# Optimization experiments

Measured on AMD Instinct MI355X. Metric: run time of the kernel, lower is better.

## Reference

```python
import jax, jax.numpy as jnp
import numpy as np

HEADS = 8
DIM_HEAD = 64
SCALE = DIM_HEAD ** -0.5


def setup_inputs() -> dict:
    key = jax.random.key(0)
    ks = jax.random.split(key, 5)
    B, N, M, D = 8, 1024, 1024, 512
    inner = HEADS * DIM_HEAD  # 512
    return {
        "x": jax.random.normal(ks[0], (B, N, D), dtype=jnp.float32),
        "context": jax.random.normal(ks[1], (B, M, D), dtype=jnp.float32),
        "Wq": jax.random.normal(ks[2], (D, inner), dtype=jnp.float32) * (D ** -0.5),
        "Wkv": jax.random.normal(ks[3], (D, 2 * inner), dtype=jnp.float32) * (D ** -0.5),
        "Wo": jax.random.normal(ks[4], (inner, D), dtype=jnp.float32) * (inner ** -0.5),
        "bo": jnp.zeros((D,), dtype=jnp.float32),
    }


def reference(x, context, Wq, Wkv, Wo, bo):
    B, N, D = x.shape
    M = context.shape[1]
    q = x @ Wq                      # [B, N, inner]
    kv = context @ Wkv              # [B, M, 2*inner]
    k, v = jnp.split(kv, 2, axis=-1)
    # b n (h d) -> b h n d
    split_heads = lambda t: t.reshape(t.shape[0], t.shape[1], HEADS, DIM_HEAD).transpose(0, 2, 1, 3)
    q, k, v = split_heads(q), split_heads(k), split_heads(v)
    dots = jnp.einsum('bhid,bhjd->bhij', q, k) * SCALE  # [B, H, N, M]
    attn = jax.nn.softmax(dots, axis=-1)
    out = jnp.einsum('bhij,bhjd->bhid', attn, v)        # [B, H, N, d]
    out = out.transpose(0, 2, 1, 3).reshape(B, N, HEADS * DIM_HEAD)
    return out @ Wo + bo            # [B, N, D]
```

## Files before the change

### kernel.cpp

```cpp
#include <hip/hip_runtime.h>
#include <stdint.h>

#define LOG2E 1.44269504088896340736f
#define QSCALE (0.125f * LOG2E)

typedef __bf16 bf16x8 __attribute__((ext_vector_type(8)));
typedef float floatx4 __attribute__((ext_vector_type(4)));

__device__ __forceinline__ unsigned short bfbits(float f) {
  __bf16 h = (__bf16)f;
  return __builtin_bit_cast(unsigned short, h);
}

__device__ __forceinline__ float fast_exp2(float x) {
#if __has_builtin(__builtin_amdgcn_exp2f)
  return __builtin_amdgcn_exp2f(x);
#else
  return exp2f(x);
#endif
}

__device__ __forceinline__ void gl2lds16(const void* g, void* l) {
  __builtin_amdgcn_global_load_lds((const __attribute__((address_space(1))) void*)g,
                                   (__attribute__((address_space(3))) void*)l, 16, 0, 0);
}

__global__ __launch_bounds__(256)
void prep_kernel(const float* __restrict__ x, const float* __restrict__ ctx,
                 const float* __restrict__ Wq, const float* __restrict__ Wkv,
                 const float* __restrict__ Wo,
                 unsigned short* __restrict__ Xb, unsigned short* __restrict__ Cb,
                 unsigned short* __restrict__ WqT, unsigned short* __restrict__ WkvT,
                 unsigned short* __restrict__ WoT) {
  int blk = blockIdx.x;
  int tid = threadIdx.x;
  if (blk < 8192) {
    const float* in = blk < 4096 ? x : ctx;
    unsigned short* out = blk < 4096 ? Xb : Cb;
    int i = (((blk & 4095) * 256) + tid) * 4;
    float4 v = *(const float4*)(in + i);
    unsigned long long pk = (unsigned long long)bfbits(v.x)
                          | ((unsigned long long)bfbits(v.y) << 16)
                          | ((unsigned long long)bfbits(v.z) << 32)
                          | ((unsigned long long)bfbits(v.w) << 48);
    *(unsigned long long*)(out + i) = pk;
  } else {
    __shared__ float tile[32][33];
    int t = blk - 8192;
    const float* in; unsigned short* out; int N; int tb;
    if (t < 256)      { in = Wq;  out = WqT;  N = 512;  tb = t; }
    else if (t < 768) { in = Wkv; out = WkvT; N = 1024; tb = t - 256; }
    else              { in = Wo;  out = WoT;  N = 512;  tb = t - 768; }
    const int K = 512;
    int nbx = N / 32;
    int n0 = (tb % nbx) * 32, k0 = (tb / nbx) * 32;
    int tx = tid & 31, ty = tid >> 5;
#pragma unroll
    for (int r = ty; r < 32; r += 8)
      tile[r][tx] = in[(long)(k0 + r) * N + n0 + tx];
    __syncthreads();
#pragma unroll
    for (int r = ty; r < 32; r += 8)
      out[(long)(n0 + r) * K + k0 + tx] = bfbits(tile[tx][r]);
  }
}

__global__ __launch_bounds__(256)
void proj_gemm(const unsigned short* __restrict__ Xb, const unsigned short* __restrict__ Cb,
               const unsigned short* __restrict__ WqT, const unsigned short* __restrict__ WkvT,
               unsigned short* __restrict__ Qb, unsigned short* __restrict__ Kb,
               unsigned short* __restrict__ Vt) {
  __shared__ unsigned short As[128 * 32];
  __shared__ unsigned short Bs[128 * 32];

  int idx = blockIdx.x;
  const unsigned short* A; const unsigned short* Bt;
  long bm, bn; int role;
  if (idx < 256) { role = 0; A = Xb; Bt = WqT;  bn = (long)(idx & 3) * 128; bm = (long)(idx >> 2) * 128; }
  else { idx -= 256; role = 1; A = Cb; Bt = WkvT; bn = (long)(idx & 7) * 128; bm = (long)(idx >> 3) * 128; }

  const int tid = threadIdx.x;
  const int wave = tid >> 6;
  const int lane = tid & 63;
  const int l15 = lane & 15;
  const int q4 = lane >> 4;
  const int wm = (wave & 1) * 64;
  const int wn = (wave >> 1) * 64;
  const int K = 512;

  floatx4 acc[4][4];
#pragma unroll
  for (int i = 0; i < 4; ++i)
#pragma unroll
    for (int j = 0; j < 4; ++j) { acc[i][j][0]=0.f; acc[i][j][1]=0.f; acc[i][j][2]=0.f; acc[i][j][3]=0.f; }

  for (int k0 = 0; k0 < K; k0 += 32) {
#pragma unroll
    for (int cc = 0; cc < 2; ++cc) {
      int c = cc * 256 + tid;
      int r = c >> 2, kc = c & 3;
      gl2lds16(A + (bm + r) * (long)K + k0 + kc * 8, (char*)As + c * 16);
      gl2lds16(Bt + (bn + r) * (long)K + k0 + kc * 8, (char*)Bs + c * 16);
    }
    __syncthreads();
    bf16x8 af[4], bfr[4];
#pragma unroll
    for (int i = 0; i < 4; ++i)
      af[i] = *(const bf16x8*)(As + (wm + i * 16 + l15) * 32 + q4 * 8);
#pragma unroll
    for (int j = 0; j < 4; ++j)
      bfr[j] = *(const bf16x8*)(Bs + (wn + j * 16 + l15) * 32 + q4 * 8);
#pragma unroll
    for (int i = 0; i < 4; ++i)
#pragma unroll
      for (int j = 0; j < 4; ++j)
        acc[i][j] = __builtin_amdgcn_mfma_f32_16x16x32_bf16(af[i], bfr[j], acc[i][j], 0, 0, 0);
    __syncthreads();
  }

  const bool vrole = (role == 1) && (bn >= 512);
#pragma unroll
  for (int i = 0; i < 4; ++i) {
#pragma unroll
    for (int j = 0; j < 4; ++j) {
      long col = bn + wn + j * 16 + l15;
      if (vrole) {
        long h = (col - 512) >> 6, d = col & 63;
        long row0 = bm + wm + i * 16 + q4 * 4;
        long b = row0 >> 10, m0 = row0 & 1023;
        unsigned long long pk = (unsigned long long)bfbits(acc[i][j][0])
                              | ((unsigned long long)bfbits(acc[i][j][1]) << 16)
                              | ((unsigned long long)bfbits(acc[i][j][2]) << 32)
                              | ((unsigned long long)bfbits(acc[i][j][3]) << 48);
        *(unsigned long long*)(Vt + ((b * 8 + h) * 64 + d) * 1024 + m0) = pk;
      } else {
        long h = col >> 6, d = col & 63;
#pragma unroll
        for (int r = 0; r < 4; ++r) {
          long row = bm + wm + i * 16 + q4 * 4 + r;
          long b = row >> 10, n = row & 1023;
          float v = acc[i][j][r];
          if (role == 0) Qb[((b * 8 + h) * 1024 + n) * 64 + d] = bfbits(v * QSCALE);
          else           Kb[((b * 8 + h) * 1024 + n) * 64 + d] = bfbits(v);
        }
      }
    }
  }
}

__global__ __launch_bounds__(256)
void attn_kernel(const unsigned short* __restrict__ Qb,
                 const unsigned short* __restrict__ Kb,
                 const unsigned short* __restrict__ Vt,
                 unsigned short* __restrict__ Ob)
{
  __shared__ unsigned short Ksm[2][4096];
  __shared__ unsigned short Vsm[2][4096];
  __shared__ unsigned short Psm[128 * 64];

  const int tid = threadIdx.x;
  const int wave = tid >> 6;
  const int lane = tid & 63;
  const int l15 = lane & 15;
  const int q4 = lane >> 4;
  const int bh = blockIdx.x;
  const int nb = blockIdx.y;

  const long qrow0 = (long)bh * 1024 + nb * 128 + wave * 32;

  bf16x8 qf[2][2];
#pragma unroll
  for (int qn = 0; qn < 2; ++qn)
#pragma unroll
    for (int ks = 0; ks < 2; ++ks)
      qf[qn][ks] = *(const bf16x8*)(Qb + (qrow0 + qn * 16 + l15) * 64 + ks * 32 + q4 * 8);

  floatx4 acc[2][4];
#pragma unroll
  for (int i = 0; i < 2; ++i)
#pragma unroll
    for (int d = 0; d < 4; ++d) { acc[i][d][0]=0.f; acc[i][d][1]=0.f; acc[i][d][2]=0.f; acc[i][d][3]=0.f; }
  float suml[2] = {0.0f, 0.0f};

  const unsigned short* Kbase = Kb + (long)bh * 65536;
  const unsigned short* Vbase = Vt + (long)bh * 65536;
  int koff[2], voff[2], lds16[2];
#pragma unroll
  for (int cc = 0; cc < 2; ++cc) {
    int c = cc * 256 + tid;
    int jrow = c >> 3;
    int cact = (c & 7) ^ (jrow & 7);
    koff[cc] = jrow * 64 + cact * 8;
    voff[cc] = jrow * 1024 + cact * 8;
    lds16[cc] = c * 16;
  }

  const int s7 = l15 & 7;
  int kfo[2][4];
  int pao[2][2];
  int pwo[2][4];
#pragma unroll
  for (int ks = 0; ks < 2; ++ks) {
#pragma unroll
    for (int jn = 0; jn < 4; ++jn)
      kfo[ks][jn] = (jn * 16 + l15) * 64 + (((ks * 4 + q4) ^ s7) * 8);
#pragma unroll
    for (int i = 0; i < 2; ++i)
      pao[ks][i] = (wave * 32 + i * 16 + l15) * 64 + (((ks * 4 + q4) ^ s7) * 8);
  }
#pragma unroll
  for (int qn = 0; qn < 2; ++qn)
#pragma unroll
    for (int jn = 0; jn < 4; ++jn)
      pwo[qn][jn] = (wave * 32 + qn * 16 + l15) * 64 + (((jn * 2 + (q4 >> 1)) ^ s7) * 8) + (q4 & 1) * 4;

#pragma unroll
  for (int cc = 0; cc < 2; ++cc) {
    gl2lds16(Kbase + koff[cc], (char*)Ksm[0] + lds16[cc]);
    gl2lds16(Vbase + voff[cc], (char*)Vsm[0] + lds16[cc]);
  }

#define ATTN_TILE(TIDX, CUR, STAGE)                                                          \
  {                                                                                          \
    __syncthreads();                                                                         \
    if (STAGE) {                                                                             \
      _Pragma("unroll")                                                                      \
      for (int cc = 0; cc < 2; ++cc) {                                                       \
        gl2lds16(Kbase + ((TIDX) + 1) * 4096 + koff[cc], (char*)Ksm[(CUR) ^ 1] + lds16[cc]); \
        gl2lds16(Vbase + ((TIDX) + 1) * 64 + voff[cc], (char*)Vsm[(CUR) ^ 1] + lds16[cc]);   \
      }                                                                                      \
    }                                                                                        \
    floatx4 st[4][2];                                                                        \
    _Pragma("unroll")                                                                        \
    for (int jn = 0; jn < 4; ++jn)                                                           \
      _Pragma("unroll")                                                                      \
      for (int qn = 0; qn < 2; ++qn) {                                                       \
        st[jn][qn][0] = 0.f; st[jn][qn][1] = 0.f; st[jn][qn][2] = 0.f; st[jn][qn][3] = 0.f;  \
      }                                                                                      \
    _Pragma("unroll")                                                                        \
    for (int ks = 0; ks < 2; ++ks) {                                                         \
      bf16x8 kfr[4];                                                                         \
      _Pragma("unroll")                                                                      \
      for (int jn = 0; jn < 4; ++jn)                                                         \
        kfr[jn] = *(const bf16x8*)(Ksm[(CUR)] + kfo[ks][jn]);                                \
      _Pragma("unroll")                                                                      \
      for (int jn = 0; jn < 4; ++jn)                                                         \
        _Pragma("unroll")                                                                    \
        for (int qn = 0; qn < 2; ++qn)                                                       \
          st[jn][qn] = __builtin_amdgcn_mfma_f32_16x16x32_bf16(kfr[jn], qf[qn][ks],          \
                                                               st[jn][qn], 0, 0, 0);         \
    }                                                                                        \
    _Pragma("unroll")                                                                        \
    for (int qn = 0; qn < 2; ++qn) {                                                         \
      _Pragma("unroll")                                                                      \
      for (int jn = 0; jn < 4; ++jn) {                                                       \
        float p0 = fast_exp2(st[jn][qn][0]);                                                 \
        float p1 = fast_exp2(st[jn][qn][1]);                                                 \
        float p2 = fast_exp2(st[jn][qn][2]);                                                 \
        float p3 = fast_exp2(st[jn][qn][3]);                                                 \
        suml[qn] += (p0 + p1) + (p2 + p3);                                                   \
        unsigned int lo = (unsigned int)bfbits(p0) | ((unsigned int)bfbits(p1) << 16);       \
        unsigned int hi = (unsigned int)bfbits(p2) | ((unsigned int)bfbits(p3) << 16);       \
        unsigned long long pk = (unsigned long long)lo | ((unsigned long long)hi << 32);     \
        *(unsigned long long*)(Psm + pwo[qn][jn]) = pk;                                      \
      }                                                                                      \
    }                                                                                        \
    __asm__ volatile("s_waitcnt lgkmcnt(0)" ::: "memory");                                   \
    _Pragma("unroll")                                                                        \
    for (int ks = 0; ks < 2; ++ks) {                                                         \
      bf16x8 pa[2], vb[4];                                                                   \
      _Pragma("unroll")                                                                      \
      for (int i = 0; i < 2; ++i)                                                            \
        pa[i] = *(const bf16x8*)(Psm + pao[ks][i]);                                          \
      _Pragma("unroll")                                                                      \
      for (int dn = 0; dn < 4; ++dn)                                                         \
        vb[dn] = *(const bf16x8*)(Vsm[(CUR)] + kfo[ks][dn]);                                 \
      _Pragma("unroll")                                                                      \
      for (int i = 0; i < 2; ++i)                                                            \
        _Pragma("unroll")                                                                    \
        for (int dn = 0; dn < 4; ++dn)                                                       \
          acc[i][dn] = __builtin_amdgcn_mfma_f32_16x16x32_bf16(pa[i], vb[dn],                \
                                                               acc[i][dn], 0, 0, 0);         \
    }                                                                                        \
  }

  for (int tt = 0; tt < 8; ++tt) {
    ATTN_TILE(2 * tt, 0, true);
    ATTN_TILE(2 * tt + 1, 1, (tt < 7));
  }
#undef ATTN_TILE

  float inv[2], invr[2][4];
#pragma unroll
  for (int qn = 0; qn < 2; ++qn) {
    float l = suml[qn];
    l += __shfl_xor(l, 16, 64);
    l += __shfl_xor(l, 32, 64);
    inv[qn] = 1.0f / l;
#pragma unroll
    for (int r = 0; r < 4; ++r) invr[qn][r] = __shfl(inv[qn], q4 * 4 + r, 64);
  }

  const int b = bh >> 3, h = bh & 7;
#pragma unroll
  for (int i = 0; i < 2; ++i) {
#pragma unroll
    for (int dn = 0; dn < 4; ++dn) {
#pragma unroll
      for (int r = 0; r < 4; ++r) {
        long row = (long)b * 1024 + nb * 128 + wave * 32 + i * 16 + q4 * 4 + r;
        long col = h * 64 + dn * 16 + l15;
        Ob[row * 512 + col] = bfbits(acc[i][dn][r] * invr[i][r]);
      }
    }
  }
}

__global__ __launch_bounds__(256)
void out_gemm(const unsigned short* __restrict__ A,
              const unsigned short* __restrict__ Bt,
              float* __restrict__ outF, const float* __restrict__ bias) {
  __shared__ unsigned short As[64 * 32];
  __shared__ unsigned short Bs[128 * 32];

  const int tid = threadIdx.x;
  const int wave = tid >> 6;
  const int lane = tid & 63;
  const int l15 = lane & 15;
  const int q4 = lane >> 4;
  const int wm = (wave & 1) * 32;
  const int wn = (wave >> 1) * 64;
  const long bm = (long)blockIdx.y * 64;
  const long bn = (long)blockIdx.x * 128;
  const int K = 512, N = 512;

  floatx4 acc[2][4];
#pragma unroll
  for (int i = 0; i < 2; ++i)
#pragma unroll
    for (int j = 0; j < 4; ++j) { acc[i][j][0]=0.f; acc[i][j][1]=0.f; acc[i][j][2]=0.f; acc[i][j][3]=0.f; }

  for (int k0 = 0; k0 < K; k0 += 32) {
    {
      int r = tid >> 2, kc = tid & 3;
      gl2lds16(A + (bm + r) * (long)K + k0 + kc * 8, (char*)As + tid * 16);
    }
#pragma unroll
    for (int cc = 0; cc < 2; ++cc) {
      int c = cc * 256 + tid;
      int r = c >> 2, kc = c & 3;
      gl2lds16(Bt + (bn + r) * (long)K + k0 + kc * 8, (char*)Bs + c * 16);
    }
    __syncthreads();
    bf16x8 af[2], bfr[4];
#pragma unroll
    for (int i = 0; i < 2; ++i)
      af[i] = *(const bf16x8*)(As + (wm + i * 16 + l15) * 32 + q4 * 8);
#pragma unroll
    for (int j = 0; j < 4; ++j)
      bfr[j] = *(const bf16x8*)(Bs + (wn + j * 16 + l15) * 32 + q4 * 8);
#pragma unroll
    for (int i = 0; i < 2; ++i)
#pragma unroll
      for (int j = 0; j < 4; ++j)
        acc[i][j] = __builtin_amdgcn_mfma_f32_16x16x32_bf16(af[i], bfr[j], acc[i][j], 0, 0, 0);
    __syncthreads();
  }

#pragma unroll
  for (int i = 0; i < 2; ++i) {
#pragma unroll
    for (int j = 0; j < 4; ++j) {
      long col = bn + wn + j * 16 + l15;
      float bv = bias[col];
#pragma unroll
      for (int r = 0; r < 4; ++r) {
        long row = bm + wm + i * 16 + q4 * 4 + r;
        outF[row * (long)N + col] = acc[i][j][r] + bv;
      }
    }
  }
}

extern "C" void kernel_launch(void* const* d_in, const int* in_sizes, int n_in,
                              void* d_out, int out_size, void* d_ws, size_t ws_size,
                              hipStream_t stream) {
  const float* x   = (const float*)d_in[0];
  const float* ctx = (const float*)d_in[1];
  const float* Wq  = (const float*)d_in[2];
  const float* Wkv = (const float*)d_in[3];
  const float* Wo  = (const float*)d_in[4];
  const float* bo  = (const float*)d_in[5];
  float* out = (float*)d_out;

  char* ws = (char*)d_ws;
  unsigned short* Xb   = (unsigned short*)(ws);
  unsigned short* Cb   = (unsigned short*)(ws + (8u  << 20));
  unsigned short* WqT  = (unsigned short*)(ws + (16u << 20));
  unsigned short* WkvT = (unsigned short*)(ws + (17u << 20));
  unsigned short* WoT  = (unsigned short*)(ws + (19u << 20));
  unsigned short* Qb   = (unsigned short*)(ws + (20u << 20));
  unsigned short* Kb   = (unsigned short*)(ws + (28u << 20));
  unsigned short* Vt   = (unsigned short*)(ws + (36u << 20));
  unsigned short* Ob   = (unsigned short*)(ws + (44u << 20));

  prep_kernel<<<9216, 256, 0, stream>>>(x, ctx, Wq, Wkv, Wo, Xb, Cb, WqT, WkvT, WoT);
  proj_gemm<<<768, 256, 0, stream>>>(Xb, Cb, WqT, WkvT, Qb, Kb, Vt);
  attn_kernel<<<dim3(64, 8), 256, 0, stream>>>(Qb, Kb, Vt, Ob);
  out_gemm<<<dim3(4, 128), 256, 0, stream>>>(Ob, WoT, out, bo);
}
```

Baseline: 153.5 us.

## Fuse fp32-to-bf16 activation conversion into projection GEMM A-tile loads

Drops the separate elementwise conversion of x and context to bf16 in the prep kernel. The projection GEMM now loads fp32 A tiles straight into LDS through an XOR-swizzled layout and converts them to bf16 in registers before the MFMA. This removes a full write-then-read round trip of both activation tensors through global memory. In exchange the GEMM moves twice as many bytes per A tile, uses more LDS, and does extra conversion work in its inner loop.

```diff
diff --git a/kernel.cpp b/kernel.cpp
--- a/kernel.cpp
+++ b/kernel.cpp
@@ -26,58 +26,43 @@
 }
 
 __global__ __launch_bounds__(256)
-void prep_kernel(const float* __restrict__ x, const float* __restrict__ ctx,
-                 const float* __restrict__ Wq, const float* __restrict__ Wkv,
+void prep_kernel(const float* __restrict__ Wq, const float* __restrict__ Wkv,
                  const float* __restrict__ Wo,
-                 unsigned short* __restrict__ Xb, unsigned short* __restrict__ Cb,
                  unsigned short* __restrict__ WqT, unsigned short* __restrict__ WkvT,
                  unsigned short* __restrict__ WoT) {
-  int blk = blockIdx.x;
+  __shared__ float tile[32][33];
+  int t = blockIdx.x;
   int tid = threadIdx.x;
-  if (blk < 8192) {
-    const float* in = blk < 4096 ? x : ctx;
-    unsigned short* out = blk < 4096 ? Xb : Cb;
-    int i = (((blk & 4095) * 256) + tid) * 4;
-    float4 v = *(const float4*)(in + i);
-    unsigned long long pk = (unsigned long long)bfbits(v.x)
-                          | ((unsigned long long)bfbits(v.y) << 16)
-                          | ((unsigned long long)bfbits(v.z) << 32)
-                          | ((unsigned long long)bfbits(v.w) << 48);
-    *(unsigned long long*)(out + i) = pk;
-  } else {
-    __shared__ float tile[32][33];
-    int t = blk - 8192;
-    const float* in; unsigned short* out; int N; int tb;
-    if (t < 256)      { in = Wq;  out = WqT;  N = 512;  tb = t; }
-    else if (t < 768) { in = Wkv; out = WkvT; N = 1024; tb = t - 256; }
-    else              { in = Wo;  out = WoT;  N = 512;  tb = t - 768; }
-    const int K = 512;
-    int nbx = N / 32;
-    int n0 = (tb % nbx) * 32, k0 = (tb / nbx) * 32;
-    int tx = tid & 31, ty = tid >> 5;
-#pragma unroll
-    for (int r = ty; r < 32; r += 8)
-      tile[r][tx] = in[(long)(k0 + r) * N + n0 + tx];
-    __syncthreads();
-#pragma unroll
-    for (int r = ty; r < 32; r += 8)
-      out[(long)(n0 + r) * K + k0 + tx] = bfbits(tile[tx][r]);
-  }
+  const float* in; unsigned short* out; int N; int tb;
+  if (t < 256)      { in = Wq;  out = WqT;  N = 512;  tb = t; }
+  else if (t < 768) { in = Wkv; out = WkvT; N = 1024; tb = t - 256; }
+  else              { in = Wo;  out = WoT;  N = 512;  tb = t - 768; }
+  const int K = 512;
+  int nbx = N / 32;
+  int n0 = (tb % nbx) * 32, k0 = (tb / nbx) * 32;
+  int tx = tid & 31, ty = tid >> 5;
+#pragma unroll
+  for (int r = ty; r < 32; r += 8)
+    tile[r][tx] = in[(long)(k0 + r) * N + n0 + tx];
+  __syncthreads();
+#pragma unroll
+  for (int r = ty; r < 32; r += 8)
+    out[(long)(n0 + r) * K + k0 + tx] = bfbits(tile[tx][r]);
 }
 
 __global__ __launch_bounds__(256)
-void proj_gemm(const unsigned short* __restrict__ Xb, const unsigned short* __restrict__ Cb,
+void proj_gemm(const float* __restrict__ Xf, const float* __restrict__ Cf,
                const unsigned short* __restrict__ WqT, const unsigned short* __restrict__ WkvT,
                unsigned short* __restrict__ Qb, unsigned short* __restrict__ Kb,
                unsigned short* __restrict__ Vt) {
-  __shared__ unsigned short As[128 * 32];
+  __shared__ float Asf[128 * 32];
   __shared__ unsigned short Bs[128 * 32];
 
   int idx = blockIdx.x;
-  const unsigned short* A; const unsigned short* Bt;
+  const float* A; const unsigned short* Bt;
   long bm, bn; int role;
-  if (idx < 256) { role = 0; A = Xb; Bt = WqT;  bn = (long)(idx & 3) * 128; bm = (long)(idx >> 2) * 128; }
-  else { idx -= 256; role = 1; A = Cb; Bt = WkvT; bn = (long)(idx & 7) * 128; bm = (long)(idx >> 3) * 128; }
+  if (idx < 256) { role = 0; A = Xf; Bt = WqT;  bn = (long)(idx & 3) * 128; bm = (long)(idx >> 2) * 128; }
+  else { idx -= 256; role = 1; A = Cf; Bt = WkvT; bn = (long)(idx & 7) * 128; bm = (long)(idx >> 3) * 128; }
 
   const int tid = threadIdx.x;
   const int wave = tid >> 6;
@@ -88,6 +73,23 @@
   const int wn = (wave >> 1) * 64;
   const int K = 512;
 
+  int aro[4], alo[4];
+#pragma unroll
+  for (int cc = 0; cc < 4; ++cc) {
+    int c = cc * 256 + tid;
+    int r = c >> 3;
+    int gact = (c & 7) ^ (r & 7);
+    aro[cc] = r * K + gact * 4;
+    alo[cc] = c * 16;
+  }
+  int afo[4][2];
+#pragma unroll
+  for (int i = 0; i < 4; ++i) {
+    int r = wm + i * 16 + l15;
+    afo[i][0] = r * 32 + (((2 * q4) ^ (r & 7)) * 4);
+    afo[i][1] = r * 32 + (((2 * q4 + 1) ^ (r & 7)) * 4);
+  }
+
   floatx4 acc[4][4];
 #pragma unroll
   for (int i = 0; i < 4; ++i)
@@ -95,18 +97,26 @@
     for (int j = 0; j < 4; ++j) { acc[i][j][0]=0.f; acc[i][j][1]=0.f; acc[i][j][2]=0.f; acc[i][j][3]=0.f; }
 
   for (int k0 = 0; k0 < K; k0 += 32) {
+#pragma unroll
+    for (int cc = 0; cc < 4; ++cc)
+      gl2lds16(A + bm * K + k0 + aro[cc], (char*)Asf + alo[cc]);
 #pragma unroll
     for (int cc = 0; cc < 2; ++cc) {
       int c = cc * 256 + tid;
       int r = c >> 2, kc = c & 3;
-      gl2lds16(A + (bm + r) * (long)K + k0 + kc * 8, (char*)As + c * 16);
       gl2lds16(Bt + (bn + r) * (long)K + k0 + kc * 8, (char*)Bs + c * 16);
     }
     __syncthreads();
     bf16x8 af[4], bfr[4];
 #pragma unroll
-    for (int i = 0; i < 4; ++i)
-      af[i] = *(const bf16x8*)(As + (wm + i * 16 + l15) * 32 + q4 * 8);
+    for (int i = 0; i < 4; ++i) {
+      float4 a0 = *(const float4*)(Asf + afo[i][0]);
+      float4 a1 = *(const float4*)(Asf + afo[i][1]);
+      bf16x8 v;
+      v[0] = (__bf16)a0.x; v[1] = (__bf16)a0.y; v[2] = (__bf16)a0.z; v[3] = (__bf16)a0.w;
+      v[4] = (__bf16)a1.x; v[5] = (__bf16)a1.y; v[6] = (__bf16)a1.z; v[7] = (__bf16)a1.w;
+      af[i] = v;
+    }
 #pragma unroll
     for (int j = 0; j < 4; ++j)
       bfr[j] = *(const bf16x8*)(Bs + (wn + j * 16 + l15) * 32 + q4 * 8);
@@ -196,9 +206,7 @@
   }
 
   const int s7 = l15 & 7;
-  int kfo[2][4];
-  int pao[2][2];
-  int pwo[2][4];
+  int kfo[2][4], pao[2][2], pwo[2][4];
 #pragma unroll
   for (int ks = 0; ks < 2; ++ks) {
 #pragma unroll
@@ -394,18 +402,16 @@
   float* out = (float*)d_out;
 
   char* ws = (char*)d_ws;
-  unsigned short* Xb   = (unsigned short*)(ws);
-  unsigned short* Cb   = (unsigned short*)(ws + (8u  << 20));
-  unsigned short* WqT  = (unsigned short*)(ws + (16u << 20));
-  unsigned short* WkvT = (unsigned short*)(ws + (17u << 20));
-  unsigned short* WoT  = (unsigned short*)(ws + (19u << 20));
-  unsigned short* Qb   = (unsigned short*)(ws + (20u << 20));
-  unsigned short* Kb   = (unsigned short*)(ws + (28u << 20));
-  unsigned short* Vt   = (unsigned short*)(ws + (36u << 20));
-  unsigned short* Ob   = (unsigned short*)(ws + (44u << 20));
-
-  prep_kernel<<<9216, 256, 0, stream>>>(x, ctx, Wq, Wkv, Wo, Xb, Cb, WqT, WkvT, WoT);
-  proj_gemm<<<768, 256, 0, stream>>>(Xb, Cb, WqT, WkvT, Qb, Kb, Vt);
+  unsigned short* WqT  = (unsigned short*)(ws);
+  unsigned short* WkvT = (unsigned short*)(ws + (1u  << 20));
+  unsigned short* WoT  = (unsigned short*)(ws + (2u  << 20));
+  unsigned short* Qb   = (unsigned short*)(ws + (4u  << 20));
+  unsigned short* Kb   = (unsigned short*)(ws + (12u << 20));
+  unsigned short* Vt   = (unsigned short*)(ws + (20u << 20));
+  unsigned short* Ob   = (unsigned short*)(ws + (28u << 20));
+
+  prep_kernel<<<1024, 256, 0, stream>>>(Wq, Wkv, Wo, WqT, WkvT, WoT);
+  proj_gemm<<<768, 256, 0, stream>>>(x, ctx, WqT, WkvT, Qb, Kb, Vt);
   attn_kernel<<<dim3(64, 8), 256, 0, stream>>>(Qb, Kb, Vt, Ob);
   out_gemm<<<dim3(4, 128), 256, 0, stream>>>(Ob, WoT, out, bo);
 }
```

After: 158.2 us. +3.0%, slower.
